# Optimization experiments

Hardware: AMD Instinct MI355X
Metric: run time of the kernel (lower is better)

The kernel has to match this reference:

```python
import jax, jax.numpy as jnp
import numpy as np

B, T, N, D = 4, 8, 256, 1024
DH, KD, VD, IM, KC, H, L = 768, 576, 1152, 2048, 4, 12, 5
DK, DV = KD // H, VD // H

def _rms(x, w, eps=1e-6):
    return x * jax.lax.rsqrt(jnp.mean(x * x, -1, keepdims=True) + eps) * w

def _l2(x, eps=1e-6):
    return x * jax.lax.rsqrt(jnp.sum(x * x, -1, keepdims=True) + eps)

def _conv_silu(x, w):
    # depthwise causal conv1d over tokens: x [b,n,C], w [C,K]
    K = w.shape[1]
    xp = jnp.pad(x, ((0, 0), (K - 1, 0), (0, 0)))
    y = sum(xp[:, j:j + x.shape[1], :] * w[:, j] for j in range(K))
    return jax.nn.silu(y)

def _gdn_attn(x, p):
    b, n, _ = x.shape
    q = _l2(_conv_silu(x @ p['wq'].T, p['cq']).reshape(b, n, H, DK))
    k = _l2(_conv_silu(x @ p['wk'].T, p['ck']).reshape(b, n, H, DK))
    v = _conv_silu(x @ p['wv'].T, p['cv']).reshape(b, n, H, DV)
    beta = jax.nn.sigmoid(x @ p['wb'].T)                                   # [b,n,H]
    g = -jnp.exp(p['A_log']) * jax.nn.softplus(x @ p['wa'].T + p['dt_bias'])  # mamba-style log-decay
    scale = DK ** -0.5

    def step(S, inp):
        qt, kt, vt, gt, bt = inp
        S = S * jnp.exp(gt)[..., None, None]                               # [b,H,dk,dv] gated decay
        v_old = jnp.einsum('bhk,bhkv->bhv', kt, S)
        dv = bt[..., None] * (vt - v_old)                                  # delta rule update
        S = S + kt[..., None] * dv[:, :, None, :]
        o = jnp.einsum('bhk,bhkv->bhv', qt, S)
        return S, o

    xs = (jnp.moveaxis(q * scale, 1, 0), jnp.moveaxis(k, 1, 0), jnp.moveaxis(v, 1, 0),
          jnp.moveaxis(g, 1, 0), jnp.moveaxis(beta, 1, 0))
    S0 = jnp.zeros((b, H, DK, DV), x.dtype)
    _, o = jax.lax.scan(step, S0, xs)
    o = jnp.moveaxis(o, 0, 1)                                              # [b,n,H,dv]
    gate = (x @ p['wg'].T).reshape(b, n, H, DV)
    o = _rms(o, p['onorm']) * gate * jax.nn.sigmoid(gate)                  # RMSNorm + swish gate
    return o.reshape(b, n, VD) @ p['wo'].T

def _block(x, p):
    x = x + _gdn_attn(_rms(x, p['n1']), p)
    h = _rms(x, p['n2'])
    return x + (jax.nn.silu(h @ p['w1'].T) * (h @ p['w3'].T)) @ p['w2'].T

def _forward(z, actions, enc_w, enc_b, ap_w, ap_b, temb, ln_w, ln_b, dec_w, dec_b, lp, block_fn):
    zt = z.reshape(B, T, N, D)
    feat = zt @ enc_w.T + enc_b                                            # 1x1 conv == per-token linear
    act = jnp.broadcast_to(actions[:, :, None, :], (B, T, N, actions.shape[-1]))
    tok = jnp.concatenate([feat, act], -1) @ ap_w.T + ap_b
    tpos = jnp.minimum(jnp.arange(T), temb.shape[0] - 1)
    tok = tok + temb[tpos][None, :, None, :]
    x = tok.reshape(B * T, N, DH)                                          # timesteps independent -> fold into batch
    for i in range(L):
        p = {k: v[i] for k, v in lp.items()}
        x = block_fn(x, p)
    mu = jnp.mean(x, -1, keepdims=True)
    var = jnp.mean((x - mu) ** 2, -1, keepdims=True)
    x = (x - mu) * jax.lax.rsqrt(var + 1e-5) * ln_w + ln_b                 # final LayerNorm
    delta = x @ dec_w.T + dec_b
    return (zt + delta.reshape(B, T, N, D)).reshape(B, T * N, D)

def setup_inputs():
    key = jax.random.key(0)
    cnt = [0]
    def nrm(shape, s=0.02):
        cnt[0] += 1
        return jax.random.normal(jax.random.fold_in(key, cnt[0]), shape, jnp.float32) * s
    A = 2
    return dict(
        z=nrm((B, T * N, D), 1.0), actions=nrm((B, T, A), 1.0),
        enc_w=nrm((DH, D)), enc_b=jnp.zeros((DH,), jnp.float32),
        ap_w=nrm((DH, DH + A)), ap_b=jnp.zeros((DH,), jnp.float32),
        temb=nrm((T + 1, DH)),
        ln_w=jnp.ones((DH,), jnp.float32), ln_b=jnp.zeros((DH,), jnp.float32),
        dec_w=nrm((D, DH)), dec_b=jnp.zeros((D,), jnp.float32),
        n1=jnp.ones((L, DH), jnp.float32), n2=jnp.ones((L, DH), jnp.float32),
        wq=nrm((L, KD, DH)), cq=nrm((L, KD, KC), 0.3),
        wk=nrm((L, KD, DH)), ck=nrm((L, KD, KC), 0.3),
        wv=nrm((L, VD, DH)), cv=nrm((L, VD, KC), 0.3),
        wb=nrm((L, H, DH)), wa=nrm((L, H, DH)),
        A_log=jnp.log(jax.random.uniform(jax.random.fold_in(key, 777), (L, H), jnp.float32, 1.0, 16.0)),
        dt_bias=nrm((L, H), 0.1),
        wg=nrm((L, VD, DH)), onorm=jnp.ones((L, DV), jnp.float32),
        wo=nrm((L, DH, VD)),
        w1=nrm((L, IM, DH)), w2=nrm((L, DH, IM)), w3=nrm((L, IM, DH)),
    )

def reference(z, actions, enc_w, enc_b, ap_w, ap_b, temb, ln_w, ln_b, dec_w, dec_b,
              n1, n2, wq, cq, wk, ck, wv, cv, wb, wa, A_log, dt_bias, wg, onorm, wo, w1, w2, w3):
    lp = dict(n1=n1, n2=n2, wq=wq, cq=cq, wk=wk, ck=ck, wv=wv, cv=cv, wb=wb, wa=wa,
              A_log=A_log, dt_bias=dt_bias, wg=wg, onorm=onorm, wo=wo, w1=w1, w2=w2, w3=w3)
    return _forward(z, actions, enc_w, enc_b, ap_w, ap_b, temb, ln_w, ln_b, dec_w, dec_b, lp, _block)
```

## Files before the change

### kernel.cpp

```cpp
#include <hip/hip_runtime.h>
#include <math.h>

#define RTOT 8192
#define SEQL 256
#define DHC 768
#define KDC 576
#define VDC 1152
#define IMC 2048
#define NHC 12
#define DKC 48
#define DVC 96
#define NLAY 5

typedef float f4 __attribute__((ext_vector_type(4)));
typedef __bf16 v8bf __attribute__((ext_vector_type(8)));

__device__ __forceinline__ float sigmoidf_(float x){ return 1.0f/(1.0f+expf(-x)); }
__device__ __forceinline__ float siluf_(float x){ return x/(1.0f+expf(-x)); }

__device__ __forceinline__ void gl16(const void* g, void* l) {
    __builtin_amdgcn_global_load_lds((const __attribute__((address_space(1))) void*)g,
                                     (__attribute__((address_space(3))) void*)l, 16, 0, 0);
}
#define MFMA_BF16(a,b,c) __builtin_amdgcn_mfma_f32_16x16x32_bf16((a),(b),(c),0,0,0)

__global__ __launch_bounds__(256)
void gemm3_kernel(const __bf16* __restrict__ Ah, const __bf16* __restrict__ Al,
                  const __bf16* __restrict__ Wh, const __bf16* __restrict__ Wl,
                  int K, int ldc, int mode,
                  float* Cf, const float* bias, const float* bias2, const float* res,
                  __bf16* Ch, __bf16* Cl, const float* aux)
{
    __shared__ __bf16 sAh[128*32], sAl[128*32], sBh[128*32], sBl[128*32];
    const int tid  = threadIdx.x;
    const int m0   = blockIdx.y * 128, n0 = blockIdx.x * 128;
    const int lane = tid & 63, wv = tid >> 6;
    const int wm   = (wv & 1) * 64, wn = (wv >> 1) * 64;

    const int o0 = tid * 16, o1 = o0 + 4096;
    const int r0 = o0 >> 6, s0 = (o0 >> 4) & 3;
    const int r1 = o1 >> 6, s1 = (o1 >> 4) & 3;
    const int k0 = (s0 ^ ((r0 >> 1) & 3)) * 8;
    const int k1 = (s1 ^ ((r1 >> 1) & 3)) * 8;

    const __bf16* gA0h = Ah + (size_t)(m0 + r0) * K + k0;
    const __bf16* gA1h = Ah + (size_t)(m0 + r1) * K + k1;
    const __bf16* gA0l = Al + (size_t)(m0 + r0) * K + k0;
    const __bf16* gA1l = Al + (size_t)(m0 + r1) * K + k1;
    const __bf16* gB0h = Wh + (size_t)(n0 + r0) * K + k0;
    const __bf16* gB1h = Wh + (size_t)(n0 + r1) * K + k1;
    const __bf16* gB0l = Wl + (size_t)(n0 + r0) * K + k0;
    const __bf16* gB1l = Wl + (size_t)(n0 + r1) * K + k1;

    const int fr = lane & 15, g8 = lane >> 4;
    int aoff[4], boff[4];
    #pragma unroll
    for (int f = 0; f < 4; ++f) {
        int ra = wm + f*16 + fr;
        aoff[f] = ra*32 + (g8 ^ ((ra >> 1) & 3)) * 8;
        int rb = wn + f*16 + fr;
        boff[f] = rb*32 + (g8 ^ ((rb >> 1) & 3)) * 8;
    }

    f4 acc[4][4];
    const f4 zero4 = {0.f, 0.f, 0.f, 0.f};
    #pragma unroll
    for (int i = 0; i < 4; ++i)
        #pragma unroll
        for (int j = 0; j < 4; ++j) acc[i][j] = zero4;

    for (int kt = 0; kt < K; kt += 32) {
        gl16(gA0h + kt, (char*)sAh + o0);
        gl16(gA1h + kt, (char*)sAh + o1);
        gl16(gA0l + kt, (char*)sAl + o0);
        gl16(gA1l + kt, (char*)sAl + o1);
        gl16(gB0h + kt, (char*)sBh + o0);
        gl16(gB1h + kt, (char*)sBh + o1);
        gl16(gB0l + kt, (char*)sBl + o0);
        gl16(gB1l + kt, (char*)sBl + o1);
        __syncthreads();

        v8bf bhv[4], blv[4];
        #pragma unroll
        for (int f = 0; f < 4; ++f) {
            bhv[f] = *(const v8bf*)(sBh + boff[f]);
            blv[f] = *(const v8bf*)(sBl + boff[f]);
        }
        #pragma unroll
        for (int i = 0; i < 4; ++i) {
            v8bf ahv = *(const v8bf*)(sAh + aoff[i]);
            v8bf alv = *(const v8bf*)(sAl + aoff[i]);
            #pragma unroll
            for (int j = 0; j < 4; ++j) {
                f4 t = MFMA_BF16(alv, bhv[j], acc[i][j]);
                t    = MFMA_BF16(ahv, blv[j], t);
                acc[i][j] = MFMA_BF16(ahv, bhv[j], t);
            }
        }
        __syncthreads();
    }

    const int rb4 = (lane >> 4) * 4;
    #pragma unroll
    for (int i = 0; i < 4; ++i) {
        #pragma unroll
        for (int jf = 0; jf < 4; ++jf) {
            int col = n0 + wn + jf*16 + fr;
            #pragma unroll
            for (int j = 0; j < 4; ++j) {
                int row = m0 + wm + i*16 + rb4 + j;
                size_t idx = (size_t)row * ldc + col;
                float v = acc[i][jf][j];
                if (bias)  v += bias[col];
                if (bias2) v += bias2[(size_t)(row >> 8) * ldc + col];
                if (res)   v += res[idx];
                if (mode == 2) v = siluf_(aux[idx]) * v;
                if (mode == 0) {
                    Cf[idx] = v;
                } else {
                    __bf16 h = (__bf16)v;
                    Ch[idx] = h;
                    Cl[idx] = (__bf16)(v - (float)h);
                }
            }
        }
    }
}

__global__ __launch_bounds__(256)
void cvt_hl_kernel(const float* __restrict__ src, int ld, int cols,
                   __bf16* __restrict__ dh, __bf16* __restrict__ dl)
{
    int r = blockIdx.x;
    const float* s = src + (size_t)r * ld;
    __bf16* ph = dh + (size_t)r * cols;
    __bf16* pl = dl + (size_t)r * cols;
    for (int c = threadIdx.x; c < cols; c += 256) {
        float v = s[c];
        __bf16 h = (__bf16)v;
        ph[c] = h;
        pl[c] = (__bf16)(v - (float)h);
    }
}

__global__ __launch_bounds__(256)
void bias2_kernel(const float* __restrict__ actions, const float* __restrict__ ap_w,
                  const float* __restrict__ ap_b, const float* __restrict__ temb,
                  float* __restrict__ B2)
{
    int bt = blockIdx.x;
    int t  = bt & 7;
    float a0 = actions[bt*2], a1 = actions[bt*2+1];
    for (int c = threadIdx.x; c < DHC; c += 256)
        B2[bt*DHC + c] = ap_b[c] + temb[t*DHC + c] + a0*ap_w[c*770 + 768] + a1*ap_w[c*770 + 769];
}

__global__ __launch_bounds__(256)
void rmsnorm_kernel(const float* __restrict__ X, const float* __restrict__ w,
                    __bf16* __restrict__ Yh, __bf16* __restrict__ Yl)
{
    int row = blockIdx.x, tid = threadIdx.x;
    const float* xr = X + (size_t)row*DHC;
    float v0 = xr[tid], v1 = xr[tid+256], v2 = xr[tid+512];
    __shared__ float red[256];
    red[tid] = v0*v0 + v1*v1 + v2*v2;
    __syncthreads();
    for (int s = 128; s; s >>= 1) { if (tid < s) red[tid] += red[tid+s]; __syncthreads(); }
    float r = 1.0f/sqrtf(red[0]/768.0f + 1e-6f);
    float y0 = v0*r*w[tid], y1 = v1*r*w[tid+256], y2 = v2*r*w[tid+512];
    __bf16* ph = Yh + (size_t)row*DHC;
    __bf16* pl = Yl + (size_t)row*DHC;
    __bf16 h0 = (__bf16)y0, h1 = (__bf16)y1, h2 = (__bf16)y2;
    ph[tid] = h0;     pl[tid]     = (__bf16)(y0 - (float)h0);
    ph[tid+256] = h1; pl[tid+256] = (__bf16)(y1 - (float)h1);
    ph[tid+512] = h2; pl[tid+512] = (__bf16)(y2 - (float)h2);
}

__global__ __launch_bounds__(256)
void layernorm_kernel(const float* __restrict__ X, const float* __restrict__ w,
                      const float* __restrict__ b, __bf16* __restrict__ Yh,
                      __bf16* __restrict__ Yl)
{
    int row = blockIdx.x, tid = threadIdx.x;
    const float* xr = X + (size_t)row*DHC;
    float v0 = xr[tid], v1 = xr[tid+256], v2 = xr[tid+512];
    __shared__ float rs[256], rs2[256];
    rs[tid]  = v0+v1+v2;
    rs2[tid] = v0*v0+v1*v1+v2*v2;
    __syncthreads();
    for (int s = 128; s; s >>= 1) { if (tid < s) { rs[tid]+=rs[tid+s]; rs2[tid]+=rs2[tid+s]; } __syncthreads(); }
    float mu  = rs[0]/768.0f;
    float var = rs2[0]/768.0f - mu*mu;
    float r = 1.0f/sqrtf(var + 1e-5f);
    float y0 = (v0-mu)*r*w[tid]     + b[tid];
    float y1 = (v1-mu)*r*w[tid+256] + b[tid+256];
    float y2 = (v2-mu)*r*w[tid+512] + b[tid+512];
    __bf16* ph = Yh + (size_t)row*DHC;
    __bf16* pl = Yl + (size_t)row*DHC;
    __bf16 h0 = (__bf16)y0, h1 = (__bf16)y1, h2 = (__bf16)y2;
    ph[tid] = h0;     pl[tid]     = (__bf16)(y0 - (float)h0);
    ph[tid+256] = h1; pl[tid+256] = (__bf16)(y1 - (float)h1);
    ph[tid+512] = h2; pl[tid+512] = (__bf16)(y2 - (float)h2);
}

__global__ __launch_bounds__(64)
void convsilu_kernel(const float* __restrict__ P, int ldp, const float* __restrict__ cw,
                     float* __restrict__ Y, int ldd, int C)
{
    int c = blockIdx.x*64 + threadIdx.x;
    if (c >= C) return;
    int r = blockIdx.y;
    int t = r & (SEQL-1);
    float acc = P[(size_t)r*ldp + c] * cw[c*4+3];
    if (t >= 1) acc += P[(size_t)(r-1)*ldp + c] * cw[c*4+2];
    if (t >= 2) acc += P[(size_t)(r-2)*ldp + c] * cw[c*4+1];
    if (t >= 3) acc += P[(size_t)(r-3)*ldp + c] * cw[c*4+0];
    Y[(size_t)r*ldd + c] = siluf_(acc);
}

__global__ __launch_bounds__(128)
void l2norm_kernel(float* __restrict__ X, int ld, int col0, float scale)
{
    int row = blockIdx.x;
    int wave = threadIdx.x >> 6, lane = threadIdx.x & 63;
    #pragma unroll
    for (int i = 0; i < 6; ++i) {
        int h = wave*6 + i;
        size_t base = (size_t)row*ld + col0 + h*DKC;
        float v = (lane < DKC) ? X[base + lane] : 0.f;
        float ss = v*v;
        for (int off = 32; off; off >>= 1) ss += __shfl_down(ss, off);
        ss = __shfl(ss, 0);
        float r = scale / sqrtf(ss + 1e-6f);
        if (lane < DKC) X[base + lane] = v*r;
    }
}

__global__ __launch_bounds__(256)
void betag_kernel(const __bf16* __restrict__ XNh, const __bf16* __restrict__ XNl,
                  const float* __restrict__ wb, const float* __restrict__ wa,
                  const float* __restrict__ Alog, const float* __restrict__ dtb,
                  float* __restrict__ Beta, float* __restrict__ Dec)
{
    int row = blockIdx.x, tid = threadIdx.x;
    __shared__ float sx[DHC];
    for (int i = tid; i < DHC; i += 256)
        sx[i] = (float)XNh[(size_t)row*DHC + i] + (float)XNl[(size_t)row*DHC + i];
    __syncthreads();
    int wave = tid >> 6, lane = tid & 63;
    for (int d = 0; d < 6; ++d) {
        int out = wave*6 + d;
        const float* wr = (out < NHC) ? (wb + out*DHC) : (wa + (out-NHC)*DHC);
        float acc = 0.f;
        for (int j = lane; j < DHC; j += 64) acc += sx[j]*wr[j];
        for (int off = 32; off; off >>= 1) acc += __shfl_down(acc, off);
        if (lane == 0) {
            if (out < NHC) {
                Beta[(size_t)row*NHC + out] = sigmoidf_(acc);
            } else {
                int h = out - NHC;
                float sp = acc + dtb[h];
                sp = (sp > 20.f) ? sp : log1pf(expf(sp));
                Dec[(size_t)row*NHC + h] = expf(-expf(Alog[h]) * sp);
            }
        }
    }
}

__global__ __launch_bounds__(384)
void scan_kernel(const float* __restrict__ QKV, const float* __restrict__ Beta,
                 const float* __restrict__ Dec, float* __restrict__ O)
{
    int bid = blockIdx.x;
    int seq = bid / NHC, h = bid % NHC;
    int tid = threadIdx.x;
    int vc = tid >> 2, rg = tid & 3;
    __shared__ float sk[DKC], sq[DKC], sv[DVC], ssc[2];

    float S[12];
    #pragma unroll
    for (int i = 0; i < 12; ++i) S[i] = 0.f;

    const float* qp = QKV + (size_t)seq*SEQL*2304 + h*DKC;
    const float* kp = qp + 576;
    const float* vp = QKV + (size_t)seq*SEQL*2304 + 1152 + h*DVC;
    const float* bp = Beta+ (size_t)seq*SEQL*NHC + h;
    const float* dp = Dec + (size_t)seq*SEQL*NHC + h;
    float* op       = O   + (size_t)seq*SEQL*VDC + h*DVC;

    for (int t = 0; t < SEQL; ++t) {
        if (tid < DKC)            sk[tid]        = kp[(size_t)t*2304 + tid];
        else if (tid < 2*DKC)     sq[tid-DKC]    = qp[(size_t)t*2304 + tid - DKC];
        else if (tid < 2*DKC+DVC) sv[tid-2*DKC]  = vp[(size_t)t*2304 + tid - 2*DKC];
        else if (tid == 200)      ssc[0] = dp[(size_t)t*NHC];
        else if (tid == 201)      ssc[1] = bp[(size_t)t*NHC];
        __syncthreads();
        float dec = ssc[0], beta = ssc[1];
        float pv = 0.f;
        #pragma unroll
        for (int i = 0; i < 12; ++i) { S[i] *= dec; pv += sk[rg*12+i]*S[i]; }
        pv += __shfl_xor(pv, 1); pv += __shfl_xor(pv, 2);
        float dvv = beta * (sv[vc] - pv);
        float po = 0.f;
        #pragma unroll
        for (int i = 0; i < 12; ++i) { S[i] += sk[rg*12+i]*dvv; po += sq[rg*12+i]*S[i]; }
        po += __shfl_xor(po, 1); po += __shfl_xor(po, 2);
        if (rg == 0) op[(size_t)t*VDC + vc] = po;
        __syncthreads();
    }
}

__global__ __launch_bounds__(128)
void opost_kernel(const float* __restrict__ O, const float* __restrict__ G, int ldg,
                  const float* __restrict__ onorm, __bf16* __restrict__ Oh,
                  __bf16* __restrict__ Ol)
{
    int row = blockIdx.x;
    int wave = threadIdx.x >> 6, lane = threadIdx.x & 63;
    #pragma unroll
    for (int i = 0; i < 6; ++i) {
        int h = wave*6 + i;
        size_t baseO = (size_t)row*VDC + h*DVC;
        size_t baseG = (size_t)row*ldg + h*DVC;
        float a = O[baseO + lane];
        float c = (lane < 32) ? O[baseO + 64 + lane] : 0.f;
        float ss = a*a + c*c;
        for (int off = 32; off; off >>= 1) ss += __shfl_down(ss, off);
        ss = __shfl(ss, 0);
        float r = 1.0f/sqrtf(ss/96.0f + 1e-6f);
        float ga = G[baseG + lane];
        float v0 = a*r*onorm[lane]*ga*sigmoidf_(ga);
        { __bf16 hh = (__bf16)v0; Oh[baseO+lane] = hh; Ol[baseO+lane] = (__bf16)(v0 - (float)hh); }
        if (lane < 32) {
            float gb = G[baseG + 64 + lane];
            float v1 = c*r*onorm[64+lane]*gb*sigmoidf_(gb);
            __bf16 hh = (__bf16)v1; Oh[baseO+64+lane] = hh; Ol[baseO+64+lane] = (__bf16)(v1 - (float)hh);
        }
    }
}

static inline void gemm3(const __bf16* Ah, const __bf16* Al, const __bf16* Wh, const __bf16* Wl,
                         int K, int ldc, int mode, float* Cf, const float* bias,
                         const float* bias2, const float* res, __bf16* Ch, __bf16* Cl,
                         const float* aux, hipStream_t s)
{
    dim3 grid(ldc/128, RTOT/128);
    hipLaunchKernelGGL(gemm3_kernel, grid, dim3(256), 0, s, Ah, Al, Wh, Wl, K, ldc, mode,
                       Cf, bias, bias2, res, Ch, Cl, aux);
}

static inline void cvt(const float* src, int ld, int rows, int cols, __bf16* dh, __bf16* dl,
                       hipStream_t s)
{
    hipLaunchKernelGGL(cvt_hl_kernel, dim3(rows), dim3(256), 0, s, src, ld, cols, dh, dl);
}

extern "C" void kernel_launch(void* const* d_in, const int* in_sizes, int n_in,
                              void* d_out, int out_size, void* d_ws, size_t ws_size,
                              hipStream_t stream)
{
    const float* z       = (const float*)d_in[0];
    const float* actions = (const float*)d_in[1];
    const float* enc_w   = (const float*)d_in[2];
    const float* enc_b   = (const float*)d_in[3];
    const float* ap_w    = (const float*)d_in[4];
    const float* ap_b    = (const float*)d_in[5];
    const float* temb    = (const float*)d_in[6];
    const float* ln_w    = (const float*)d_in[7];
    const float* ln_b    = (const float*)d_in[8];
    const float* dec_w   = (const float*)d_in[9];
    const float* dec_b   = (const float*)d_in[10];
    const float* n1      = (const float*)d_in[11];
    const float* n2      = (const float*)d_in[12];
    const float* wq      = (const float*)d_in[13];
    const float* cq      = (const float*)d_in[14];
    const float* wk      = (const float*)d_in[15];
    const float* ck      = (const float*)d_in[16];
    const float* wv      = (const float*)d_in[17];
    const float* cv      = (const float*)d_in[18];
    const float* wb      = (const float*)d_in[19];
    const float* wa      = (const float*)d_in[20];
    const float* A_log   = (const float*)d_in[21];
    const float* dt_bias = (const float*)d_in[22];
    const float* wg      = (const float*)d_in[23];
    const float* onorm   = (const float*)d_in[24];
    const float* wo      = (const float*)d_in[25];
    const float* w1      = (const float*)d_in[26];
    const float* w2      = (const float*)d_in[27];
    const float* w3      = (const float*)d_in[28];

    const size_t R = RTOT;
    const float qscale = 0.14433756729740643f;

    float* X    = (float*)d_ws;
    float* BUF1 = X    + 768*R;
    float* O    = BUF1 + 1152*R;
    float* QKV  = O    + 1152*R;
    float* BETA = QKV  + 2304*R;
    float* DEC  = BETA + 12*R;
    float* TMP  = DEC  + 12*R;
    __bf16* XNh = (__bf16*)(TMP + 32*768);
    __bf16* XNl = XNh + 768*R;
    __bf16* WS0 = XNl + 768*R;

    const size_t need = (size_t)(768+1152+1152+2304+24)*R*4 + 32*768*4
                      + ((size_t)1536*R + 16515072)*2;
    if (ws_size < need) return;

    __bf16* zh  = (__bf16*)QKV;
    __bf16* zl  = zh + 1024*R;
    __bf16* Oh  = (__bf16*)QKV;
    __bf16* Ol  = Oh + 1152*R;
    float*  A1f = QKV;
    __bf16* A1h = (__bf16*)BUF1;
    __bf16* A1l = (__bf16*)O;

    {
        __bf16* ench = WS0;                       __bf16* encl = ench + (size_t)768*1024;
        __bf16* aph  = encl + (size_t)768*1024;   __bf16* apl  = aph  + (size_t)768*768;
        cvt(z,     1024, RTOT, 1024, zh,   zl,   stream);
        cvt(enc_w, 1024, 768,  1024, ench, encl, stream);
        cvt(ap_w,  770,  768,  768,  aph,  apl,  stream);
        hipLaunchKernelGGL(bias2_kernel, dim3(32), dim3(256), 0, stream, actions, ap_w, ap_b, temb, TMP);
        gemm3(zh, zl, ench, encl, 1024, 768, 1, nullptr, enc_b, nullptr, nullptr, XNh, XNl, nullptr, stream);
        gemm3(XNh, XNl, aph, apl, 768, 768, 0, X, nullptr, TMP, nullptr, nullptr, nullptr, nullptr, stream);
    }

    for (int l = 0; l < NLAY; ++l) {
        __bf16* qkh = WS0;                        __bf16* qkl = qkh + (size_t)1152*768;
        __bf16* vh  = qkl + (size_t)1152*768;     __bf16* vl  = vh  + (size_t)1152*768;
        __bf16* gh  = vl  + (size_t)1152*768;     __bf16* gl_ = gh  + (size_t)1152*768;
        __bf16* woh = gl_ + (size_t)1152*768;     __bf16* wol = woh + (size_t)768*1152;
        __bf16* w1h = wol + (size_t)768*1152;     __bf16* w1l = w1h + (size_t)2048*768;
        __bf16* w3h = w1l + (size_t)2048*768;     __bf16* w3l = w3h + (size_t)2048*768;
        __bf16* w2h = w3l + (size_t)2048*768;     __bf16* w2l = w2h + (size_t)768*2048;

        cvt(wq + (size_t)l*KDC*DHC, 768, 576,  768,  qkh,                  qkl,                  stream);
        cvt(wk + (size_t)l*KDC*DHC, 768, 576,  768,  qkh + (size_t)576*768, qkl + (size_t)576*768, stream);
        cvt(wv + (size_t)l*VDC*DHC, 768, 1152, 768,  vh,  vl,  stream);
        cvt(wg + (size_t)l*VDC*DHC, 768, 1152, 768,  gh,  gl_, stream);
        cvt(wo + (size_t)l*DHC*VDC, 1152, 768, 1152, woh, wol, stream);
        cvt(w1 + (size_t)l*IMC*DHC, 768, 2048, 768,  w1h, w1l, stream);
        cvt(w3 + (size_t)l*IMC*DHC, 768, 2048, 768,  w3h, w3l, stream);
        cvt(w2 + (size_t)l*DHC*IMC, 2048, 768, 2048, w2h, w2l, stream);

        hipLaunchKernelGGL(rmsnorm_kernel, dim3(RTOT), dim3(256), 0, stream, X, n1 + l*DHC, XNh, XNl);

        gemm3(XNh, XNl, qkh, qkl, 768, 1152, 0, BUF1, nullptr, nullptr, nullptr, nullptr, nullptr, nullptr, stream);
        hipLaunchKernelGGL(convsilu_kernel, dim3(9,  RTOT), dim3(64), 0, stream, BUF1,       1152, cq + (size_t)l*KDC*4, QKV,        2304, KDC);
        hipLaunchKernelGGL(convsilu_kernel, dim3(9,  RTOT), dim3(64), 0, stream, BUF1 + 576, 1152, ck + (size_t)l*KDC*4, QKV + 576,  2304, KDC);
        gemm3(XNh, XNl, vh, vl, 768, 1152, 0, BUF1, nullptr, nullptr, nullptr, nullptr, nullptr, nullptr, stream);
        hipLaunchKernelGGL(convsilu_kernel, dim3(18, RTOT), dim3(64), 0, stream, BUF1,       1152, cv + (size_t)l*VDC*4, QKV + 1152, 2304, VDC);
        gemm3(XNh, XNl, gh, gl_, 768, 1152, 0, BUF1, nullptr, nullptr, nullptr, nullptr, nullptr, nullptr, stream);
        hipLaunchKernelGGL(betag_kernel, dim3(RTOT), dim3(256), 0, stream,
                           XNh, XNl, wb + (size_t)l*NHC*DHC, wa + (size_t)l*NHC*DHC,
                           A_log + l*NHC, dt_bias + l*NHC, BETA, DEC);

        hipLaunchKernelGGL(l2norm_kernel, dim3(RTOT), dim3(128), 0, stream, QKV, 2304, 0,   qscale);
        hipLaunchKernelGGL(l2norm_kernel, dim3(RTOT), dim3(128), 0, stream, QKV, 2304, 576, 1.0f);

        hipLaunchKernelGGL(scan_kernel, dim3(32*NHC), dim3(384), 0, stream, QKV, BETA, DEC, O);

        hipLaunchKernelGGL(opost_kernel, dim3(RTOT), dim3(128), 0, stream, O, BUF1, 1152,
                           onorm + l*DVC, Oh, Ol);
        gemm3(Oh, Ol, woh, wol, 1152, 768, 0, X, nullptr, nullptr, X, nullptr, nullptr, nullptr, stream);

        hipLaunchKernelGGL(rmsnorm_kernel, dim3(RTOT), dim3(256), 0, stream, X, n2 + l*DHC, XNh, XNl);
        gemm3(XNh, XNl, w1h, w1l, 768, 2048, 0, A1f, nullptr, nullptr, nullptr, nullptr, nullptr, nullptr, stream);
        gemm3(XNh, XNl, w3h, w3l, 768, 2048, 2, nullptr, nullptr, nullptr, nullptr, A1h, A1l, A1f, stream);
        gemm3(A1h, A1l, w2h, w2l, 2048, 768, 0, X, nullptr, nullptr, X, nullptr, nullptr, nullptr, stream);
    }

    {
        __bf16* dech = WS0;  __bf16* decl = dech + (size_t)1024*768;
        cvt(dec_w, 768, 1024, 768, dech, decl, stream);
        hipLaunchKernelGGL(layernorm_kernel, dim3(RTOT), dim3(256), 0, stream, X, ln_w, ln_b, XNh, XNl);
        gemm3(XNh, XNl, dech, decl, 768, 1024, 0, (float*)d_out, dec_b, nullptr, z, nullptr, nullptr, nullptr, stream);
    }
}
```

Baseline: 6.528 ms.

## Prefetch scan inputs into double-buffered LDS and batch weight conversions

The recurrent scan kernel now double-buffers its per-step q/k/v/decay/beta inputs in shared memory. Each thread prefetches timestep t+2 into a register while step t computes, which removes one of the two barriers per step and hides global-load latency on the serial chain. The accumulation is also split into two partial sums to shorten dependency chains. Separately, the many per-matrix fp32-to-bf16 hi/lo conversion launches are merged into one batched launch per layer, cutting launch overhead at the cost of a small per-block job lookup.

```diff
diff --git a/kernel.cpp b/kernel.cpp
--- a/kernel.cpp
+++ b/kernel.cpp
@@ -127,19 +127,32 @@
     }
 }
 
+struct CvtBatch8 {
+    const float* src[8];
+    __bf16* dh[8];
+    __bf16* dl[8];
+    int ldv[8];
+    int cols[8];
+    int rowend[8];
+};
+
 __global__ __launch_bounds__(256)
-void cvt_hl_kernel(const float* __restrict__ src, int ld, int cols,
-                   __bf16* __restrict__ dh, __bf16* __restrict__ dl)
+void cvt_batch_kernel(CvtBatch8 b, int njobs)
 {
     int r = blockIdx.x;
-    const float* s = src + (size_t)r * ld;
-    __bf16* ph = dh + (size_t)r * cols;
-    __bf16* pl = dl + (size_t)r * cols;
+    int j = 0;
+    while (j < njobs - 1 && r >= b.rowend[j]) ++j;
+    int row0 = (j == 0) ? 0 : b.rowend[j-1];
+    int lr = r - row0;
+    const float* s = b.src[j] + (size_t)lr * b.ldv[j];
+    __bf16* ph = b.dh[j] + (size_t)lr * b.cols[j];
+    __bf16* pl = b.dl[j] + (size_t)lr * b.cols[j];
+    int cols = b.cols[j];
     for (int c = threadIdx.x; c < cols; c += 256) {
         float v = s[c];
-        __bf16 h = (__bf16)v;
-        ph[c] = h;
-        pl[c] = (__bf16)(v - (float)h);
+        __bf16 hh = (__bf16)v;
+        ph[c] = hh;
+        pl[c] = (__bf16)(v - (float)hh);
     }
 }
 
@@ -267,6 +280,32 @@
     }
 }
 
+#define SCAN_STEP(CUR, T)                                                   \
+    {                                                                       \
+        float dec = sbuf[CUR][192], beta = sbuf[CUR][193];                  \
+        const float* sk = &sbuf[CUR][0];                                    \
+        const float* sq = &sbuf[CUR][48];                                   \
+        const float* sv = &sbuf[CUR][96];                                   \
+        float pv0 = 0.f, pv1 = 0.f;                                         \
+        _Pragma("unroll")                                                   \
+        for (int i = 0; i < 12; i += 2) {                                   \
+            S[i]   *= dec; pv0 += sk[rg*12+i]  *S[i];                       \
+            S[i+1] *= dec; pv1 += sk[rg*12+i+1]*S[i+1];                     \
+        }                                                                   \
+        float pv = pv0 + pv1;                                               \
+        pv += __shfl_xor(pv, 1); pv += __shfl_xor(pv, 2);                   \
+        float dvv = beta * (sv[vc] - pv);                                   \
+        float po0 = 0.f, po1 = 0.f;                                         \
+        _Pragma("unroll")                                                   \
+        for (int i = 0; i < 12; i += 2) {                                   \
+            S[i]   += sk[rg*12+i]  *dvv; po0 += sq[rg*12+i]  *S[i];         \
+            S[i+1] += sk[rg*12+i+1]*dvv; po1 += sq[rg*12+i+1]*S[i+1];       \
+        }                                                                   \
+        float po = po0 + po1;                                               \
+        po += __shfl_xor(po, 1); po += __shfl_xor(po, 2);                   \
+        if (rg == 0) op[(size_t)(T)*VDC + vc] = po;                         \
+    }
+
 __global__ __launch_bounds__(384)
 void scan_kernel(const float* __restrict__ QKV, const float* __restrict__ Beta,
                  const float* __restrict__ Dec, float* __restrict__ O)
@@ -275,38 +314,55 @@
     int seq = bid / NHC, h = bid % NHC;
     int tid = threadIdx.x;
     int vc = tid >> 2, rg = tid & 3;
-    __shared__ float sk[DKC], sq[DKC], sv[DVC], ssc[2];
+    __shared__ float sbuf[2][194];
 
     float S[12];
     #pragma unroll
     for (int i = 0; i < 12; ++i) S[i] = 0.f;
 
-    const float* qp = QKV + (size_t)seq*SEQL*2304 + h*DKC;
-    const float* kp = qp + 576;
-    const float* vp = QKV + (size_t)seq*SEQL*2304 + 1152 + h*DVC;
-    const float* bp = Beta+ (size_t)seq*SEQL*NHC + h;
-    const float* dp = Dec + (size_t)seq*SEQL*NHC + h;
-    float* op       = O   + (size_t)seq*SEQL*VDC + h*DVC;
-
-    for (int t = 0; t < SEQL; ++t) {
-        if (tid < DKC)            sk[tid]        = kp[(size_t)t*2304 + tid];
-        else if (tid < 2*DKC)     sq[tid-DKC]    = qp[(size_t)t*2304 + tid - DKC];
-        else if (tid < 2*DKC+DVC) sv[tid-2*DKC]  = vp[(size_t)t*2304 + tid - 2*DKC];
-        else if (tid == 200)      ssc[0] = dp[(size_t)t*NHC];
-        else if (tid == 201)      ssc[1] = bp[(size_t)t*NHC];
-        __syncthreads();
-        float dec = ssc[0], beta = ssc[1];
-        float pv = 0.f;
-        #pragma unroll
-        for (int i = 0; i < 12; ++i) { S[i] *= dec; pv += sk[rg*12+i]*S[i]; }
-        pv += __shfl_xor(pv, 1); pv += __shfl_xor(pv, 2);
-        float dvv = beta * (sv[vc] - pv);
-        float po = 0.f;
-        #pragma unroll
-        for (int i = 0; i < 12; ++i) { S[i] += sk[rg*12+i]*dvv; po += sq[rg*12+i]*S[i]; }
-        po += __shfl_xor(po, 1); po += __shfl_xor(po, 2);
-        if (rg == 0) op[(size_t)t*VDC + vc] = po;
-        __syncthreads();
+    float* op = O + (size_t)seq*SEQL*VDC + h*DVC;
+
+    const float* gptr = QKV;
+    int gstride = 0;
+    const bool ldr = (tid < 194);
+    if (tid < 192) {
+        int col;
+        if (tid < 48)       col = 576  + h*DKC + tid;
+        else if (tid < 96)  col =        h*DKC + (tid - 48);
+        else                col = 1152 + h*DVC + (tid - 96);
+        gptr = QKV + (size_t)seq*SEQL*2304 + col;
+        gstride = 2304;
+    } else if (tid == 192) {
+        gptr = Dec  + (size_t)seq*SEQL*NHC + h;  gstride = NHC;
+    } else if (tid == 193) {
+        gptr = Beta + (size_t)seq*SEQL*NHC + h;  gstride = NHC;
+    }
+
+    float pA = 0.f, pB = 0.f;
+    if (ldr) {
+        sbuf[0][tid] = gptr[0];
+        pA = gptr[gstride];
+    }
+    __syncthreads();
+
+    int cur = 0;
+    for (int t = 0; t < SEQL; t += 2) {
+        {
+            int tn = t + 2; if (tn > SEQL-1) tn = SEQL-1;
+            if (ldr) pB = gptr[(size_t)tn * gstride];
+            SCAN_STEP(cur, t)
+            if (ldr) sbuf[cur^1][tid] = pA;
+            __syncthreads();
+            cur ^= 1;
+        }
+        {
+            int tn = t + 3; if (tn > SEQL-1) tn = SEQL-1;
+            if (ldr) pA = gptr[(size_t)tn * gstride];
+            SCAN_STEP(cur, t+1)
+            if (ldr) sbuf[cur^1][tid] = pB;
+            __syncthreads();
+            cur ^= 1;
+        }
     }
 }
 
@@ -347,12 +403,6 @@
     dim3 grid(ldc/128, RTOT/128);
     hipLaunchKernelGGL(gemm3_kernel, grid, dim3(256), 0, s, Ah, Al, Wh, Wl, K, ldc, mode,
                        Cf, bias, bias2, res, Ch, Cl, aux);
-}
-
-static inline void cvt(const float* src, int ld, int rows, int cols, __bf16* dh, __bf16* dl,
-                       hipStream_t s)
-{
-    hipLaunchKernelGGL(cvt_hl_kernel, dim3(rows), dim3(256), 0, s, src, ld, cols, dh, dl);
 }
 
 extern "C" void kernel_launch(void* const* d_in, const int* in_sizes, int n_in,
@@ -418,9 +468,13 @@
     {
         __bf16* ench = WS0;                       __bf16* encl = ench + (size_t)768*1024;
         __bf16* aph  = encl + (size_t)768*1024;   __bf16* apl  = aph  + (size_t)768*768;
-        cvt(z,     1024, RTOT, 1024, zh,   zl,   stream);
-        cvt(enc_w, 1024, 768,  1024, ench, encl, stream);
-        cvt(ap_w,  770,  768,  768,  aph,  apl,  stream);
+
+        CvtBatch8 eb{};
+        eb.src[0]=z;     eb.dh[0]=zh;   eb.dl[0]=zl;   eb.ldv[0]=1024; eb.cols[0]=1024; eb.rowend[0]=8192;
+        eb.src[1]=enc_w; eb.dh[1]=ench; eb.dl[1]=encl; eb.ldv[1]=1024; eb.cols[1]=1024; eb.rowend[1]=8960;
+        eb.src[2]=ap_w;  eb.dh[2]=aph;  eb.dl[2]=apl;  eb.ldv[2]=770;  eb.cols[2]=768;  eb.rowend[2]=9728;
+        hipLaunchKernelGGL(cvt_batch_kernel, dim3(9728), dim3(256), 0, stream, eb, 3);
+
         hipLaunchKernelGGL(bias2_kernel, dim3(32), dim3(256), 0, stream, actions, ap_w, ap_b, temb, TMP);
         gemm3(zh, zl, ench, encl, 1024, 768, 1, nullptr, enc_b, nullptr, nullptr, XNh, XNl, nullptr, stream);
         gemm3(XNh, XNl, aph, apl, 768, 768, 0, X, nullptr, TMP, nullptr, nullptr, nullptr, nullptr, stream);
@@ -435,14 +489,16 @@
         __bf16* w3h = w1l + (size_t)2048*768;     __bf16* w3l = w3h + (size_t)2048*768;
         __bf16* w2h = w3l + (size_t)2048*768;     __bf16* w2l = w2h + (size_t)768*2048;
 
-        cvt(wq + (size_t)l*KDC*DHC, 768, 576,  768,  qkh,                  qkl,                  stream);
-        cvt(wk + (size_t)l*KDC*DHC, 768, 576,  768,  qkh + (size_t)576*768, qkl + (size_t)576*768, stream);
-        cvt(wv + (size_t)l*VDC*DHC, 768, 1152, 768,  vh,  vl,  stream);
-        cvt(wg + (size_t)l*VDC*DHC, 768, 1152, 768,  gh,  gl_, stream);
-        cvt(wo + (size_t)l*DHC*VDC, 1152, 768, 1152, woh, wol, stream);
-        cvt(w1 + (size_t)l*IMC*DHC, 768, 2048, 768,  w1h, w1l, stream);
-        cvt(w3 + (size_t)l*IMC*DHC, 768, 2048, 768,  w3h, w3l, stream);
-        cvt(w2 + (size_t)l*DHC*IMC, 2048, 768, 2048, w2h, w2l, stream);
+        CvtBatch8 lb{};
+        lb.src[0]=wq + (size_t)l*KDC*DHC; lb.dh[0]=qkh;                   lb.dl[0]=qkl;                   lb.ldv[0]=768;  lb.cols[0]=768;  lb.rowend[0]=576;
+        lb.src[1]=wk + (size_t)l*KDC*DHC; lb.dh[1]=qkh+(size_t)576*768;   lb.dl[1]=qkl+(size_t)576*768;   lb.ldv[1]=768;  lb.cols[1]=768;  lb.rowend[1]=1152;
+        lb.src[2]=wv + (size_t)l*VDC*DHC; lb.dh[2]=vh;                    lb.dl[2]=vl;                    lb.ldv[2]=768;  lb.cols[2]=768;  lb.rowend[2]=2304;
+        lb.src[3]=wg + (size_t)l*VDC*DHC; lb.dh[3]=gh;                    lb.dl[3]=gl_;                   lb.ldv[3]=768;  lb.cols[3]=768;  lb.rowend[3]=3456;
+        lb.src[4]=wo + (size_t)l*DHC*VDC; lb.dh[4]=woh;                   lb.dl[4]=wol;                   lb.ldv[4]=1152; lb.cols[4]=1152; lb.rowend[4]=4224;
+        lb.src[5]=w1 + (size_t)l*IMC*DHC; lb.dh[5]=w1h;                   lb.dl[5]=w1l;                   lb.ldv[5]=768;  lb.cols[5]=768;  lb.rowend[5]=6272;
+        lb.src[6]=w3 + (size_t)l*IMC*DHC; lb.dh[6]=w3h;                   lb.dl[6]=w3l;                   lb.ldv[6]=768;  lb.cols[6]=768;  lb.rowend[6]=8320;
+        lb.src[7]=w2 + (size_t)l*DHC*IMC; lb.dh[7]=w2h;                   lb.dl[7]=w2l;                   lb.ldv[7]=2048; lb.cols[7]=2048; lb.rowend[7]=9088;
+        hipLaunchKernelGGL(cvt_batch_kernel, dim3(9088), dim3(256), 0, stream, lb, 8);
 
         hipLaunchKernelGGL(rmsnorm_kernel, dim3(RTOT), dim3(256), 0, stream, X, n1 + l*DHC, XNh, XNl);
 
@@ -473,7 +529,9 @@
 
     {
         __bf16* dech = WS0;  __bf16* decl = dech + (size_t)1024*768;
-        cvt(dec_w, 768, 1024, 768, dech, decl, stream);
+        CvtBatch8 db{};
+        db.src[0]=dec_w; db.dh[0]=dech; db.dl[0]=decl; db.ldv[0]=768; db.cols[0]=768; db.rowend[0]=1024;
+        hipLaunchKernelGGL(cvt_batch_kernel, dim3(1024), dim3(256), 0, stream, db, 1);
         hipLaunchKernelGGL(layernorm_kernel, dim3(RTOT), dim3(256), 0, stream, X, ln_w, ln_b, XNh, XNl);
         gemm3(XNh, XNl, dech, decl, 768, 1024, 0, (float*)d_out, dec_b, nullptr, z, nullptr, nullptr, nullptr, stream);
     }
```

New measurement: 5.884 ms. 1.11x faster.
